# Optimization experiments

Measured on AMD Instinct MI355X. Metric: run time of the kernel, lower is better.

Reference implementation:

```python
import jax, jax.numpy as jnp
import numpy as np

H = 16
D_MODEL = 1024
D_K = D_MODEL // H


def setup_inputs() -> dict:
    key = jax.random.key(0)
    kx, kq, kk, kv, ko = jax.random.split(key, 5)
    B, T = 4, 2048
    scale = 1.0 / np.sqrt(D_MODEL)
    return {
        "X": jax.random.normal(kx, (B, T, D_MODEL), dtype=jnp.float32),
        "W_q": jax.random.normal(kq, (D_MODEL, D_MODEL), dtype=jnp.float32) * scale,
        "W_k": jax.random.normal(kk, (D_MODEL, D_MODEL), dtype=jnp.float32) * scale,
        "W_v": jax.random.normal(kv, (D_MODEL, D_MODEL), dtype=jnp.float32) * scale,
        "W_o": jax.random.normal(ko, (D_MODEL, D_MODEL), dtype=jnp.float32) * scale,
    }


def reference(X, W_q, W_k, W_v, W_o):
    B, T, D = X.shape
    # projections (torch Linear: x @ W.T); weights stored as [out, in]=[D,D]
    Q = (X @ W_q.T).reshape(B, T, H, D_K).transpose(0, 2, 1, 3)  # [B,H,T,Dk]
    K = (X @ W_k.T).reshape(B, T, H, D_K).transpose(0, 2, 1, 3)
    V = (X @ W_v.T).reshape(B, T, H, D_K).transpose(0, 2, 1, 3)
    S = jnp.einsum("bhqd,bhkd->bhqk", Q, K) * (D_K ** -0.5)  # [B,H,T,T]
    causal = jnp.tril(jnp.ones((T, T), dtype=bool))
    S = jnp.where(causal, S, -jnp.inf)
    A = jax.nn.softmax(S, axis=-1)
    out = jnp.einsum("bhqk,bhkd->bhqd", A, V)  # [B,H,T,Dk]
    out = out.transpose(0, 2, 1, 3).reshape(B, T, D)
    return out @ W_o.T
```

## Files before the change

### kernel.cpp

```cpp
#include <hip/hip_runtime.h>
#include <hip/hip_bf16.h>

#define T_SEQ 2048
#define NB 4
#define NH 16
#define DK 64
#define DM 1024
#define QKS 2048

typedef __attribute__((ext_vector_type(8))) __bf16 bf16x8;
typedef __attribute__((ext_vector_type(4))) __bf16 bf16x4;
typedef __attribute__((ext_vector_type(4))) float f32x4;
typedef __attribute__((ext_vector_type(2))) int i32x2;
typedef __attribute__((ext_vector_type(4))) int i32x4;

__device__ __forceinline__ void gl_lds16(const __bf16* g, __bf16* l) {
  __builtin_amdgcn_global_load_lds(
      (const __attribute__((address_space(1))) void*)g,
      (__attribute__((address_space(3))) void*)l,
      16, 0, 0);
}

__device__ __forceinline__ unsigned cvt_pk_bf16(float lo, float hi) {
  unsigned r;
  asm("v_cvt_pk_bf16_f32 %0, %1, %2" : "=v"(r) : "v"(lo), "v"(hi));
  return r;
}

__global__ __launch_bounds__(256) void cast_f32_to_bf16(const float* __restrict__ in,
                                                        __bf16* __restrict__ out, int n4) {
  int i = blockIdx.x * 256 + threadIdx.x;
  if (i >= n4) return;
  float4 v = reinterpret_cast<const float4*>(in)[i];
  bf16x4 o;
  o[0] = (__bf16)v.x; o[1] = (__bf16)v.y; o[2] = (__bf16)v.z; o[3] = (__bf16)v.w;
  reinterpret_cast<bf16x4*>(out)[i] = o;
}

__global__ __launch_bounds__(256) void cast_weights(const float* __restrict__ a,
                                                    const float* __restrict__ b,
                                                    const float* __restrict__ c,
                                                    const float* __restrict__ d,
                                                    __bf16* __restrict__ oa,
                                                    __bf16* __restrict__ ob,
                                                    __bf16* __restrict__ oc,
                                                    __bf16* __restrict__ od) {
  const int which = blockIdx.y;
  const float* in = (which == 0) ? a : (which == 1) ? b : (which == 2) ? c : d;
  __bf16* out = (which == 0) ? oa : (which == 1) ? ob : (which == 2) ? oc : od;
  int i = blockIdx.x * 256 + threadIdx.x;
  float4 v = reinterpret_cast<const float4*>(in)[i];
  bf16x4 o;
  o[0] = (__bf16)v.x; o[1] = (__bf16)v.y; o[2] = (__bf16)v.z; o[3] = (__bf16)v.w;
  reinterpret_cast<bf16x4*>(out)[i] = o;
}

template<typename CT, int MODE>
__global__ __launch_bounds__(256, 2) void gemm_nt(const __bf16* __restrict__ A,
                                                  const __bf16* __restrict__ B,
                                                  CT* __restrict__ C,
                                                  int M, int N, int K) {
  __shared__ alignas(16) __bf16 As[128][64];
  __shared__ alignas(16) __bf16 Bs[128][64];
  const int tid = threadIdx.x;
  const int m0 = blockIdx.y * 128, n0 = blockIdx.x * 128;
  const int w = tid >> 6, l = tid & 63, lg = l >> 4, lr = l & 15;
  const int wr = (w >> 1) * 64, wc = (w & 1) * 64;
  const int srow = l >> 3;
  const int schunk = (l & 7) ^ srow;

  f32x4 acc[4][4] = {};
  const int rsw = lr & 7;

  for (int k0 = 0; k0 < K; k0 += 64) {
    __syncthreads();
    #pragma unroll
    for (int j = 0; j < 4; ++j) {
      const int rbase = (w * 4 + j) * 8;
      gl_lds16(A + (size_t)(m0 + rbase + srow) * K + k0 + schunk * 8, &As[rbase][0]);
      gl_lds16(B + (size_t)(n0 + rbase + srow) * K + k0 + schunk * 8, &Bs[rbase][0]);
    }
    asm volatile("s_waitcnt vmcnt(0)" ::: "memory");
    __syncthreads();
    #pragma unroll
    for (int kk = 0; kk < 2; ++kk) {
      bf16x8 af[4], bfr[4];
      #pragma unroll
      for (int mt = 0; mt < 4; ++mt) {
        const char* p = (const char*)&As[wr + mt * 16 + lr][0];
        af[mt] = *reinterpret_cast<const bf16x8*>(p + (((kk * 4 + lg) ^ rsw) << 4));
      }
      #pragma unroll
      for (int nt = 0; nt < 4; ++nt) {
        const char* p = (const char*)&Bs[wc + nt * 16 + lr][0];
        bfr[nt] = *reinterpret_cast<const bf16x8*>(p + (((kk * 4 + lg) ^ rsw) << 4));
      }
      __builtin_amdgcn_s_setprio(1);
      #pragma unroll
      for (int mt = 0; mt < 4; ++mt)
        #pragma unroll
        for (int nt = 0; nt < 4; ++nt)
          acc[mt][nt] = __builtin_amdgcn_mfma_f32_16x16x32_bf16(af[mt], bfr[nt], acc[mt][nt], 0, 0, 0);
      __builtin_amdgcn_s_setprio(0);
    }
  }
  const float qsc = (MODE == 1 && n0 < 1024) ? 0.18033688f : 1.0f;
  #pragma unroll
  for (int mt = 0; mt < 4; ++mt)
    #pragma unroll
    for (int nt = 0; nt < 4; ++nt)
      #pragma unroll
      for (int r = 0; r < 4; ++r) {
        const int mg = m0 + wr + mt * 16 + 4 * lg + r;
        int ng = n0 + wc + nt * 16 + lr;
        if (MODE == 2)
          ng = (ng & ~31) | (8 * (lr >> 2) + (lr & 3) + ((nt & 1) << 2));
        float v = acc[mt][nt][r];
        if (MODE == 1) v *= qsc;
        C[(size_t)mg * N + ng] = (CT)v;
      }
}

__global__ __launch_bounds__(256, 2) void attn_fwd(const __bf16* __restrict__ QK,
                                                   const __bf16* __restrict__ VT,
                                                   __bf16* __restrict__ AO) {
  __shared__ alignas(16) __bf16 Ks[2][64][64];
  __shared__ alignas(16) __bf16 Vs[2][64][64];
  const int tid = threadIdx.x;
  const int w = tid >> 6, l = tid & 63, lg = l >> 4, lr = l & 15;

  const int fl = (int)blockIdx.x + 8 * (int)blockIdx.y;
  const int bh = ((fl & 7) << 3) | ((fl >> 3) & 7);
  const int c = fl >> 6;
  const int b = bh >> 4, h = bh & 15;
  const size_t bT = (size_t)b * T_SEQ;
  const int M = NB * T_SEQ;

  const int srow = l >> 3;
  const int schunk = (l & 7) ^ srow;
  const __bf16* Kg = QK + bT * QKS + 1024 + h * DK;
  const __bf16* Vg = VT + (size_t)(h * DK) * M + bT;
  const int rsw = lr & 7;

  bf16x8 vone;
  #pragma unroll
  for (int j = 0; j < 8; ++j) vone[j] = (__bf16)1.0f;

  const int qbA = c, qbB = 15 - c, qbC = 16 + c, qbD = 31 - c;
  const int qrwA = qbA * 64 + w * 16, qrwB = qbB * 64 + w * 16;
  const int qrwC = qbC * 64 + w * 16, qrwD = qbD * 64 + w * 16;
  const int klA = qbA * 64, klB = qbB * 64, klC = qbC * 64, klD = qbD * 64;

  const __bf16* QpA = QK + (bT + qrwA + lr) * QKS + h * DK;
  const __bf16* QpB = QK + (bT + qrwB + lr) * QKS + h * DK;
  const __bf16* QpC = QK + (bT + qrwC + lr) * QKS + h * DK;
  const __bf16* QpD = QK + (bT + qrwD + lr) * QKS + h * DK;
  const bf16x8 qfA0 = *reinterpret_cast<const bf16x8*>(QpA + 8 * lg);
  const bf16x8 qfA1 = *reinterpret_cast<const bf16x8*>(QpA + 32 + 8 * lg);
  const bf16x8 qfB0 = *reinterpret_cast<const bf16x8*>(QpB + 8 * lg);
  const bf16x8 qfB1 = *reinterpret_cast<const bf16x8*>(QpB + 32 + 8 * lg);
  const bf16x8 qfC0 = *reinterpret_cast<const bf16x8*>(QpC + 8 * lg);
  const bf16x8 qfC1 = *reinterpret_cast<const bf16x8*>(QpC + 32 + 8 * lg);
  const bf16x8 qfD0 = *reinterpret_cast<const bf16x8*>(QpD + 8 * lg);
  const bf16x8 qfD1 = *reinterpret_cast<const bf16x8*>(QpD + 32 + 8 * lg);

  f32x4 o_accA[4] = {}, o_accB[4] = {}, o_accC[4] = {}, o_accD[4] = {};
  f32x4 lA = {}, lB = {}, lC = {}, lD = {};

  auto STAGE = [&](int buf, int kbase) {
    #pragma unroll
    for (int i = 0; i < 2; ++i) {
      const int seg = w * 2 + i;
      gl_lds16(Kg + (size_t)(kbase + seg * 8 + srow) * QKS + schunk * 8,
               &Ks[buf][seg * 8][0]);
      gl_lds16(Vg + (size_t)(seg * 8 + srow) * M + kbase + schunk * 8,
               &Vs[buf][seg * 8][0]);
    }
  };

  auto CHUNK = [&](const bf16x8& qf0, const bf16x8& qf1, f32x4* o_acc,
                   f32x4& l_acc, int qrw, bool masked, int k0,
                   const bf16x8* kf, const bf16x8* vf) {
    f32x4 s[4] = {};
    __builtin_amdgcn_s_setprio(1);
    #pragma unroll
    for (int ct = 0; ct < 4; ++ct) {
      s[ct] = __builtin_amdgcn_mfma_f32_16x16x32_bf16(kf[2 * ct], qf0, s[ct], 0, 0, 0);
      s[ct] = __builtin_amdgcn_mfma_f32_16x16x32_bf16(kf[2 * ct + 1], qf1, s[ct], 0, 0, 0);
    }
    __builtin_amdgcn_s_setprio(0);
    if (masked) {
      #pragma unroll
      for (int ct = 0; ct < 4; ++ct)
        #pragma unroll
        for (int r = 0; r < 4; ++r)
          if (k0 + 16 * ct + 4 * lg + r > qrw + lr) s[ct][r] = -1e30f;
    }
    unsigned pk[4][2];
    #pragma unroll
    for (int ct = 0; ct < 4; ++ct) {
      const float p0 = __builtin_amdgcn_exp2f(s[ct][0]);
      const float p1 = __builtin_amdgcn_exp2f(s[ct][1]);
      const float p2 = __builtin_amdgcn_exp2f(s[ct][2]);
      const float p3 = __builtin_amdgcn_exp2f(s[ct][3]);
      pk[ct][0] = cvt_pk_bf16(p0, p1);
      pk[ct][1] = cvt_pk_bf16(p2, p3);
    }
    const bf16x8 pf0 = __builtin_bit_cast(bf16x8, i32x4{(int)pk[0][0], (int)pk[0][1],
                                                        (int)pk[1][0], (int)pk[1][1]});
    const bf16x8 pf1 = __builtin_bit_cast(bf16x8, i32x4{(int)pk[2][0], (int)pk[2][1],
                                                        (int)pk[3][0], (int)pk[3][1]});
    __builtin_amdgcn_s_setprio(1);
    l_acc = __builtin_amdgcn_mfma_f32_16x16x32_bf16(pf0, vone, l_acc, 0, 0, 0);
    l_acc = __builtin_amdgcn_mfma_f32_16x16x32_bf16(pf1, vone, l_acc, 0, 0, 0);
    #pragma unroll
    for (int dt = 0; dt < 4; ++dt) {
      o_acc[dt] = __builtin_amdgcn_mfma_f32_16x16x32_bf16(pf0, vf[2 * dt],     o_acc[dt], 0, 0, 0);
      o_acc[dt] = __builtin_amdgcn_mfma_f32_16x16x32_bf16(pf1, vf[2 * dt + 1], o_acc[dt], 0, 0, 0);
    }
    __builtin_amdgcn_s_setprio(0);
  };

  STAGE(0, 0);
  asm volatile("s_waitcnt vmcnt(0)" ::: "memory");
  __syncthreads();
  int buf = 0;

  for (int k0 = 0; k0 <= klD; k0 += 64) {
    if (k0 + 64 <= klD) STAGE(buf ^ 1, k0 + 64);

    bf16x8 kf[8], vf[8];
    #pragma unroll
    for (int ct = 0; ct < 4; ++ct) {
      const char* kb = (const char*)&Ks[buf][ct * 16 + lr][0];
      kf[2 * ct]     = *reinterpret_cast<const bf16x8*>(kb + ((lg ^ rsw) << 4));
      kf[2 * ct + 1] = *reinterpret_cast<const bf16x8*>(kb + (((lg + 4) ^ rsw) << 4));
      const char* vb = (const char*)&Vs[buf][ct * 16 + lr][0];
      vf[2 * ct]     = *reinterpret_cast<const bf16x8*>(vb + ((lg ^ rsw) << 4));
      vf[2 * ct + 1] = *reinterpret_cast<const bf16x8*>(vb + (((lg + 4) ^ rsw) << 4));
    }

    CHUNK(qfD0, qfD1, o_accD, lD, qrwD, k0 == klD, k0, kf, vf);
    if (k0 <= klC) CHUNK(qfC0, qfC1, o_accC, lC, qrwC, k0 == klC, k0, kf, vf);
    if (k0 <= klB) CHUNK(qfB0, qfB1, o_accB, lB, qrwB, k0 == klB, k0, kf, vf);
    if (k0 <= klA) CHUNK(qfA0, qfA1, o_accA, lA, qrwA, k0 == klA, k0, kf, vf);

    asm volatile("s_waitcnt vmcnt(0)" ::: "memory");
    __syncthreads();
    buf ^= 1;
  }

  #pragma unroll
  for (int cc = 0; cc < 4; ++cc) {
    const f32x4& la = (cc == 0) ? lA : (cc == 1) ? lB : (cc == 2) ? lC : lD;
    f32x4* oa = (cc == 0) ? o_accA : (cc == 1) ? o_accB : (cc == 2) ? o_accC : o_accD;
    const int qrw = (cc == 0) ? qrwA : (cc == 1) ? qrwB : (cc == 2) ? qrwC : qrwD;
    #pragma unroll
    for (int r = 0; r < 4; ++r) {
      const float inv = 1.0f / la[r];
      #pragma unroll
      for (int dt = 0; dt < 4; ++dt) {
        const int rg = qrw + 4 * lg + r;
        const int cg = h * DK + dt * 16 + lr;
        AO[(bT + rg) * DM + cg] = (__bf16)(oa[dt][r] * inv);
      }
    }
  }
}

extern "C" void kernel_launch(void* const* d_in, const int* in_sizes, int n_in,
                              void* d_out, int out_size, void* d_ws, size_t ws_size,
                              hipStream_t stream) {
  (void)in_sizes; (void)n_in; (void)out_size; (void)ws_size;
  const float* X  = (const float*)d_in[0];
  const float* Wq = (const float*)d_in[1];
  const float* Wk = (const float*)d_in[2];
  const float* Wv = (const float*)d_in[3];
  const float* Wo = (const float*)d_in[4];
  float* OUT = (float*)d_out;

  char* ws = (char*)d_ws;
  const size_t SZ_X  = (size_t)NB * T_SEQ * DM * 2;
  const size_t SZ_W  = (size_t)DM * DM * 2;
  const size_t SZ_QK = (size_t)NB * T_SEQ * QKS * 2;
  __bf16* Xb  = (__bf16*)ws; ws += SZ_X;
  __bf16* Wqb = (__bf16*)ws; ws += SZ_W;
  __bf16* Wkb = (__bf16*)ws; ws += SZ_W;
  __bf16* Wvb = (__bf16*)ws; ws += SZ_W;
  __bf16* Wob = (__bf16*)ws; ws += SZ_W;
  __bf16* QKb = (__bf16*)ws; ws += SZ_QK;
  __bf16* VTb = (__bf16*)ws; ws += SZ_X;
  __bf16* AOb = (__bf16*)ws; ws += SZ_X;

  const int M = NB * T_SEQ;

  cast_f32_to_bf16<<<(M * DM / 4) / 256, 256, 0, stream>>>(X, Xb, M * DM / 4);
  cast_weights<<<dim3(DM * DM / 4 / 256, 4), 256, 0, stream>>>(Wq, Wk, Wv, Wo,
                                                               Wqb, Wkb, Wvb, Wob);

  gemm_nt<__bf16, 1><<<dim3(QKS / 128, M / 128), 256, 0, stream>>>(Xb, Wqb, QKb, M, QKS, DM);
  gemm_nt<__bf16, 2><<<dim3(M / 128, DM / 128), 256, 0, stream>>>(Wvb, Xb, VTb, DM, M, DM);
  attn_fwd<<<dim3(8, NB * NH), 256, 0, stream>>>(QKb, VTb, AOb);
  gemm_nt<float, 0><<<dim3(DM / 128, M / 128), 256, 0, stream>>>(AOb, Wob, OUT, M, DM, DM);
}
```

Before: 146.4 us.

## Add 256x256 eight-wave pipelined GEMM for the Q/K projection

```diff
diff --git a/kernel.cpp b/kernel.cpp
--- a/kernel.cpp
+++ b/kernel.cpp
@@ -55,6 +55,139 @@
   reinterpret_cast<bf16x4*>(out)[i] = o;
 }
 
+template<int DO_QSCALE>
+__global__ __launch_bounds__(512, 2) void gemm_nt_8p(const __bf16* __restrict__ A,
+                                                     const __bf16* __restrict__ Bm,
+                                                     __bf16* __restrict__ C,
+                                                     int M, int N, int K) {
+  __shared__ alignas(16) __bf16 As[2][256][64];
+  __shared__ alignas(16) __bf16 Bs[2][256][64];
+  const int tid = threadIdx.x;
+  const int wid = tid >> 6, l = tid & 63, lg = l >> 4, lr = l & 15;
+  const int wm = wid >> 2, wn = wid & 3;
+  const int f = (int)blockIdx.x;
+  const int cpx = (int)gridDim.x >> 3;
+  const int swz = (f & 7) * cpx + (f >> 3);
+  const int nbn = N >> 8;
+  const int m0 = (swz / nbn) << 8, n0 = (swz % nbn) << 8;
+
+  const int srow = l >> 3;
+  const int schunk = (l & 7) ^ srow;
+  const int rsw = lr & 7;
+  const int strow = wid * 8 + srow;
+
+  f32x4 acc[8][4] = {};
+  bf16x8 aA[8], bB[8];
+
+  auto SA = [&](int buf, int half, int t) {
+    #pragma unroll
+    for (int j = 0; j < 2; ++j)
+      gl_lds16(A + (size_t)(m0 + half * 128 + j * 64 + strow) * K + t * 64 + schunk * 8,
+               &As[buf][half * 128 + j * 64 + wid * 8][0]);
+  };
+  auto SB = [&](int buf, int half, int t) {
+    #pragma unroll
+    for (int j = 0; j < 2; ++j)
+      gl_lds16(Bm + (size_t)(n0 + half * 128 + j * 64 + strow) * K + t * 64 + schunk * 8,
+               &Bs[buf][half * 128 + j * 64 + wid * 8][0]);
+  };
+  auto LA = [&](int buf, int mh) {
+    #pragma unroll
+    for (int mt = 0; mt < 4; ++mt) {
+      const char* p = (const char*)&As[buf][wm * 128 + mh * 64 + mt * 16 + lr][0];
+      aA[mt * 2 + 0] = *reinterpret_cast<const bf16x8*>(p + ((lg ^ rsw) << 4));
+      aA[mt * 2 + 1] = *reinterpret_cast<const bf16x8*>(p + (((4 + lg) ^ rsw) << 4));
+    }
+  };
+  auto LB = [&](int buf) {
+    #pragma unroll
+    for (int nt = 0; nt < 4; ++nt) {
+      const char* p = (const char*)&Bs[buf][wn * 64 + nt * 16 + lr][0];
+      bB[nt * 2 + 0] = *reinterpret_cast<const bf16x8*>(p + ((lg ^ rsw) << 4));
+      bB[nt * 2 + 1] = *reinterpret_cast<const bf16x8*>(p + (((4 + lg) ^ rsw) << 4));
+    }
+  };
+  auto MQ = [&](int mh, int nh) {
+    #pragma unroll
+    for (int mt = 0; mt < 4; ++mt)
+      #pragma unroll
+      for (int ntl = 0; ntl < 2; ++ntl) {
+        const int nt = nh * 2 + ntl;
+        acc[mh * 4 + mt][nt] = __builtin_amdgcn_mfma_f32_16x16x32_bf16(
+            aA[mt * 2 + 0], bB[nt * 2 + 0], acc[mh * 4 + mt][nt], 0, 0, 0);
+        acc[mh * 4 + mt][nt] = __builtin_amdgcn_mfma_f32_16x16x32_bf16(
+            aA[mt * 2 + 1], bB[nt * 2 + 1], acc[mh * 4 + mt][nt], 0, 0, 0);
+      }
+  };
+
+  SB(0, 0, 0); SB(0, 1, 0); SA(0, 0, 0); SA(0, 1, 0);
+  SB(1, 0, 1); SB(1, 1, 1); SA(1, 0, 1);
+  asm volatile("s_waitcnt vmcnt(6)" ::: "memory");
+  __builtin_amdgcn_s_barrier();
+
+  const int NIT = K >> 7;
+  for (int i = 0; i < NIT; ++i) {
+    const bool lastit = (i == NIT - 1);
+    const int t2 = 2 * i + 2, t3 = 2 * i + 3;
+    LA(0, 0); LB(0);
+    SA(1, 1, 2 * i + 1);
+    __builtin_amdgcn_s_barrier();
+    asm volatile("s_waitcnt lgkmcnt(0)" ::: "memory");
+    __builtin_amdgcn_sched_barrier(0);
+    __builtin_amdgcn_s_setprio(1); MQ(0, 0); __builtin_amdgcn_s_setprio(0);
+    __builtin_amdgcn_s_barrier();
+    if (!lastit) SB(0, 0, t2);
+    __builtin_amdgcn_s_setprio(1); MQ(0, 1); __builtin_amdgcn_s_setprio(0);
+    __builtin_amdgcn_s_barrier();
+    LA(0, 1);
+    if (!lastit) SB(0, 1, t2);
+    __builtin_amdgcn_s_barrier();
+    asm volatile("s_waitcnt lgkmcnt(0)" ::: "memory");
+    __builtin_amdgcn_sched_barrier(0);
+    __builtin_amdgcn_s_setprio(1); MQ(1, 1); __builtin_amdgcn_s_setprio(0);
+    __builtin_amdgcn_s_barrier();
+    if (!lastit) SA(0, 0, t2);
+    __builtin_amdgcn_s_setprio(1); MQ(1, 0); __builtin_amdgcn_s_setprio(0);
+    if (lastit) asm volatile("s_waitcnt vmcnt(0)" ::: "memory");
+    else        asm volatile("s_waitcnt vmcnt(6)" ::: "memory");
+    __builtin_amdgcn_s_barrier();
+    LA(1, 0); LB(1);
+    if (!lastit) SA(0, 1, t2);
+    __builtin_amdgcn_s_barrier();
+    asm volatile("s_waitcnt lgkmcnt(0)" ::: "memory");
+    __builtin_amdgcn_sched_barrier(0);
+    __builtin_amdgcn_s_setprio(1); MQ(0, 0); __builtin_amdgcn_s_setprio(0);
+    __builtin_amdgcn_s_barrier();
+    if (!lastit) SB(1, 0, t3);
+    __builtin_amdgcn_s_setprio(1); MQ(0, 1); __builtin_amdgcn_s_setprio(0);
+    __builtin_amdgcn_s_barrier();
+    LA(1, 1);
+    if (!lastit) SB(1, 1, t3);
+    __builtin_amdgcn_s_barrier();
+    asm volatile("s_waitcnt lgkmcnt(0)" ::: "memory");
+    __builtin_amdgcn_sched_barrier(0);
+    __builtin_amdgcn_s_setprio(1); MQ(1, 1); __builtin_amdgcn_s_setprio(0);
+    __builtin_amdgcn_s_barrier();
+    if (!lastit) SA(1, 0, t3);
+    __builtin_amdgcn_s_setprio(1); MQ(1, 0); __builtin_amdgcn_s_setprio(0);
+    if (!lastit) asm volatile("s_waitcnt vmcnt(6)" ::: "memory");
+    __builtin_amdgcn_s_barrier();
+  }
+
+  #pragma unroll
+  for (int mt = 0; mt < 8; ++mt)
+    #pragma unroll
+    for (int nt = 0; nt < 4; ++nt) {
+      const int ng = n0 + wn * 64 + nt * 16 + lr;
+      const float sc = (DO_QSCALE && ng < 1024) ? 0.18033688f : 1.0f;
+      #pragma unroll
+      for (int r = 0; r < 4; ++r) {
+        const int mg = m0 + wm * 128 + mt * 16 + 4 * lg + r;
+        C[(size_t)mg * N + ng] = (__bf16)(acc[mt][nt][r] * sc);
+      }
+    }
+}
+
 template<typename CT, int MODE>
 __global__ __launch_bounds__(256, 2) void gemm_nt(const __bf16* __restrict__ A,
                                                   const __bf16* __restrict__ B,
@@ -104,7 +237,6 @@
       __builtin_amdgcn_s_setprio(0);
     }
   }
-  const float qsc = (MODE == 1 && n0 < 1024) ? 0.18033688f : 1.0f;
   #pragma unroll
   for (int mt = 0; mt < 4; ++mt)
     #pragma unroll
@@ -115,9 +247,7 @@
         int ng = n0 + wc + nt * 16 + lr;
         if (MODE == 2)
           ng = (ng & ~31) | (8 * (lr >> 2) + (lr & 3) + ((nt & 1) << 2));
-        float v = acc[mt][nt][r];
-        if (MODE == 1) v *= qsc;
-        C[(size_t)mg * N + ng] = (CT)v;
+        C[(size_t)mg * N + ng] = (CT)acc[mt][nt][r];
       }
 }
 
@@ -298,7 +428,7 @@
   cast_weights<<<dim3(DM * DM / 4 / 256, 4), 256, 0, stream>>>(Wq, Wk, Wv, Wo,
                                                                Wqb, Wkb, Wvb, Wob);
 
-  gemm_nt<__bf16, 1><<<dim3(QKS / 128, M / 128), 256, 0, stream>>>(Xb, Wqb, QKb, M, QKS, DM);
+  gemm_nt_8p<1><<<(M / 256) * (QKS / 256), 512, 0, stream>>>(Xb, Wqb, QKb, M, QKS, DM);
   gemm_nt<__bf16, 2><<<dim3(M / 128, DM / 128), 256, 0, stream>>>(Wvb, Xb, VTb, DM, M, DM);
   attn_fwd<<<dim3(8, NB * NH), 256, 0, stream>>>(QKb, VTb, AOb);
   gemm_nt<float, 0><<<dim3(DM / 128, M / 128), 256, 0, stream>>>(AOb, Wob, OUT, M, DM, DM);
```

Result: faster. 143.2 us (-2.2%).
